# Kernel optimization log

Hardware: AMD Instinct MI355X
Metric: run time of the kernel (lower is better)

Reference implementation:

```python
import jax, jax.numpy as jnp
import numpy as np

B, T, C = 4, 2048, 1024
H, D = 16, 64  # num_heads, head_dim
WINDOW = 256


def setup_inputs() -> dict:
    key = jax.random.key(0)
    k_x, k_qkv, k_proj, k_qb, k_pb = jax.random.split(key, 5)
    x = jax.random.normal(k_x, (B, T, C), dtype=jnp.float32)
    # xavier-uniform-ish init for qkv weight (as in _reset_parameters)
    lim_qkv = float(np.sqrt(6.0 / (C + 3 * C)))
    qkv_w = jax.random.uniform(k_qkv, (3 * C, C), minval=-lim_qkv, maxval=lim_qkv, dtype=jnp.float32)
    qkv_b = jax.random.normal(k_qb, (3 * C,), dtype=jnp.float32) * 0.02
    lim_p = float(np.sqrt(1.0 / C))
    proj_w = jax.random.uniform(k_proj, (C, C), minval=-lim_p, maxval=lim_p, dtype=jnp.float32)
    proj_b = jax.random.normal(k_pb, (C,), dtype=jnp.float32) * 0.02
    # windowed causal mask: attend to j iff j <= i and i - j < WINDOW
    i = jnp.arange(T)[:, None]
    j = jnp.arange(T)[None, :]
    attn_mask = (j <= i) & (i - j < WINDOW)  # [T, T] bool
    return {"x": x, "attn_mask": attn_mask, "qkv_w": qkv_w, "qkv_b": qkv_b,
            "proj_w": proj_w, "proj_b": proj_b}


def reference(x, attn_mask, qkv_w, qkv_b, proj_w, proj_b):
    qkv = (x @ qkv_w.T + qkv_b).reshape(B, T, 3, H, D)
    qkv = jnp.transpose(qkv, (2, 0, 3, 1, 4))
    q, k, v = qkv[0], qkv[1], qkv[2]
    scale = 1.0 / jnp.sqrt(jnp.asarray(D, dtype=q.dtype))
    scores = jnp.einsum('bhqd,bhkd->bhqk', q, k) * scale  # [B,H,T,T]
    neg = jnp.asarray(jnp.finfo(scores.dtype).min, dtype=scores.dtype)
    scores = jnp.where(attn_mask[None, None], scores, neg)
    attn = jax.nn.softmax(scores, axis=-1)
    out = jnp.einsum('bhqk,bhkd->bhqd', attn, v)  # [B,H,T,D]
    out = jnp.transpose(out, (0, 2, 1, 3)).reshape(B, T, C)
    out = out @ proj_w.T + proj_b
    return out
```

## Files before the change

kernel.cpp:

```cpp
#include <hip/hip_runtime.h>

#define BB 4
#define TT 2048
#define CC 1024
#define HH 16
#define DD 64
#define WIN 256

typedef __attribute__((ext_vector_type(8))) short short8;
typedef __attribute__((ext_vector_type(4))) float floatx4;
typedef unsigned short u16;

typedef __attribute__((address_space(3))) void lds_void;
typedef const __attribute__((address_space(1))) void g_void;

__device__ __forceinline__ void gl_lds16(const u16* g, u16* l) {
    __builtin_amdgcn_global_load_lds((g_void*)g, (lds_void*)l, 16, 0, 0);
}

__device__ __forceinline__ float bf2f(u16 u) {
    union { unsigned int i; float f; } v; v.i = ((unsigned int)u) << 16; return v.f;
}
__device__ __forceinline__ u16 f2bf(float f) {
    union { float f; unsigned int i; } v; v.f = f;
    unsigned int x = v.i;
    x += ((x >> 16) & 1u) + 0x7FFFu;
    return (u16)(x >> 16);
}

__global__ void cvt_all(const float* __restrict__ x, const float* __restrict__ qw,
                        const float* __restrict__ pw,
                        u16* __restrict__ xb, u16* __restrict__ wb, u16* __restrict__ pwb) {
    int bid = blockIdx.x;
    const float* src; u16* dst; int off;
    if (bid < 4096)      { src = x;  dst = xb;  off = bid; }
    else if (bid < 5632) { src = qw; dst = wb;  off = bid - 4096; }
    else                 { src = pw; dst = pwb; off = bid - 5632; }
    int i = (off * 256 + (int)threadIdx.x) * 8;
    float4 a = *(const float4*)(src + i);
    float4 b = *(const float4*)(src + i + 4);
    u16 o[8] = { f2bf(a.x), f2bf(a.y), f2bf(a.z), f2bf(a.w),
                 f2bf(b.x), f2bf(b.y), f2bf(b.z), f2bf(b.w) };
    *(uint4*)(dst + i) = *(const uint4*)o;
}


#define STG(s, t) do { const int ko = (t) * 32;                              \
        gl_lds16(gA0 + ko, &lA[s][wave * 512]);                              \
        gl_lds16(gA1 + ko, &lA[s][4096 + wave * 512]);                       \
        gl_lds16(gB0 + ko, &lB[s][wave * 512]); } while (0)
#define LDAB(s) do { _Pragma("unroll")                                       \
        for (int i = 0; i < 4; ++i)                                          \
            af[i] = *(const short8*)&lA[s][(wm * 4 + i) * 512 + rdoff];      \
        _Pragma("unroll")                                                    \
        for (int j = 0; j < 4; ++j)                                          \
            bf[j] = *(const short8*)&lB[s][(wn * 4 + j) * 512 + rdoff]; } while (0)
#define MM() do { __builtin_amdgcn_s_setprio(1); _Pragma("unroll")           \
        for (int i = 0; i < 4; ++i) { _Pragma("unroll")                      \
            for (int j = 0; j < 4; ++j)                                      \
                acc[i][j] = __builtin_amdgcn_mfma_f32_16x16x32_bf16(         \
                    af[i], bf[j], acc[i][j], 0, 0, 0); }                     \
        __builtin_amdgcn_s_setprio(0); } while (0)
#define BARX() do { asm volatile("" ::: "memory");                           \
        __builtin_amdgcn_s_barrier();                                        \
        asm volatile("" ::: "memory"); } while (0)
#define VM12() asm volatile("s_waitcnt vmcnt(12)" ::: "memory")

#define GEMM_BODY                                                            \
    const int K = CC;                                                        \
    __shared__ u16 lA[6][8192];                                              \
    __shared__ u16 lB[6][4096];                                              \
    const int tid = threadIdx.x;                                             \
    const int wave = tid >> 6, lane = tid & 63;                              \
    const int wm = wave >> 1, wn = wave & 1;                                 \
    const int quad = lane >> 4, l15 = lane & 15;                             \
    const int r0 = wave * 16 + (lane >> 2);                                  \
    const int r1 = r0 + 128;                                                 \
    const int c0 = (lane & 3) ^ ((r0 >> 1) & 3);                             \
    const u16* gA0 = Amat + (size_t)(bM + r0) * K + c0 * 8;                  \
    const u16* gA1 = Amat + (size_t)(bM + r1) * K + c0 * 8;                  \
    const u16* gB0 = Bw + (size_t)(bN + r0) * K + c0 * 8;                    \
    const int rdoff = l15 * 32 + ((quad ^ ((l15 >> 1) & 3)) * 8);            \
    floatx4 acc[4][4] = {};                                                  \
    STG(0, 0); STG(1, 1); STG(2, 2); STG(3, 3); STG(4, 4);                   \
    VM12(); BARX();                                                          \
    _Pragma("unroll")                                                        \
    for (int P = 0; P < 32; ++P) {                                           \
        short8 af[4], bf[4];                                                 \
        LDAB(P % 6);                                                         \
        STG((P + 5) % 6, (P + 5 < 32) ? (P + 5) : (P - 1));                  \
        VM12(); BARX(); MM(); BARX();                                        \
    }

__global__ __launch_bounds__(512, 2) void gemm_qkv(
    const u16* __restrict__ Amat, const u16* __restrict__ Bw,
    const float* __restrict__ bias,
    u16* __restrict__ Qb, u16* __restrict__ Kb, u16* __restrict__ Vb)
{
    const int raw = blockIdx.x;
    const int xcd = raw & 7;
    const int l   = raw >> 3;
    const int bM  = (xcd * 4 + (l & 3)) * 256;
    const int bN  = (l >> 2) * 128;

    GEMM_BODY

#pragma unroll
    for (int mf = 0; mf < 4; ++mf)
#pragma unroll
        for (int nf = 0; nf < 4; ++nf) {
            int col = bN + wn * 64 + nf * 16 + l15;
            float bv = bias[col];
            int which = col >> 10, rem = col & 1023;
            int h = rem >> 6, d = rem & 63;
            u16* dst = which == 0 ? Qb : (which == 1 ? Kb : Vb);
#pragma unroll
            for (int rg = 0; rg < 4; ++rg) {
                int row = bM + wm * 64 + mf * 16 + quad * 4 + rg;
                int b = row >> 11, t = row & 2047;
                float v = acc[mf][nf][rg] + bv;
                dst[(((size_t)(b * HH + h)) * TT + t) * DD + d] = f2bf(v);
            }
        }
}

__global__ __launch_bounds__(512, 2) void gemm_proj(
    const u16* __restrict__ Amat, const u16* __restrict__ Bw,
    const float* __restrict__ bias, float* __restrict__ Out)
{
    const int raw = blockIdx.x;
    const int xcd = raw & 7;
    const int l   = raw >> 3;
    const int bM  = (xcd * 4 + (l & 3)) * 256;
    const int bN  = (l >> 2) * 128;

    GEMM_BODY

#pragma unroll
    for (int mf = 0; mf < 4; ++mf)
#pragma unroll
        for (int nf = 0; nf < 4; ++nf) {
            int col = bN + wn * 64 + nf * 16 + l15;
            float bv = bias[col];
#pragma unroll
            for (int rg = 0; rg < 4; ++rg) {
                int row = bM + wm * 64 + mf * 16 + quad * 4 + rg;
                Out[(size_t)row * CC + col] = acc[mf][nf][rg] + bv;
            }
        }
}

#undef STG
#undef LDAB
#undef MM
#undef BARX
#undef VM12
#undef GEMM_BODY

__global__ __launch_bounds__(256) void attn_mfma(
    const u16* __restrict__ Qb, const u16* __restrict__ Kb, const u16* __restrict__ Vb,
    u16* __restrict__ Y)
{
    __shared__ u16 Ks[64][72];
    __shared__ u16 Vt[64][72];
    __shared__ u16 Ps[4][16][72];

    const int tid = threadIdx.x;
    const int wave = tid >> 6, lane = tid & 63;
    const int quad = lane >> 4, l15 = lane & 15;
    const int q0 = blockIdx.x * 64;
    const int bh = blockIdx.y;
    const int b = bh >> 4, h = bh & 15;
    const u16* Qp = Qb + (size_t)bh * TT * DD;
    const u16* Kp = Kb + (size_t)bh * TT * DD;
    const u16* Vp = Vb + (size_t)bh * TT * DD;
    const int qw = q0 + wave * 16;

    short8 qf[2];
    qf[0] = *(const short8*)&Qp[(size_t)(qw + l15) * DD + quad * 8];
    qf[1] = *(const short8*)&Qp[(size_t)(qw + l15) * DD + 32 + quad * 8];

    float m_i[4] = { -1e30f, -1e30f, -1e30f, -1e30f };
    float l_i[4] = { 0.f, 0.f, 0.f, 0.f };
    floatx4 Oacc[4] = {};

    const int kb = (q0 >= WIN) ? (q0 - WIN) : 0;
    for (int j0 = kb; j0 < q0 + 64; j0 += 64) {
        __syncthreads();
#pragma unroll
        for (int it = 0; it < 2; ++it) {
            int slot = tid + it * 256;
            int j = slot >> 3, c8 = (slot & 7) << 3;
            *(uint4*)&Ks[j][c8] = *(const uint4*)&Kp[(size_t)(j0 + j) * DD + c8];
        }
#pragma unroll
        for (int it = 0; it < 2; ++it) {
            int slot = tid + it * 256;
            int j = slot >> 3, d0 = (slot & 7) << 3;
            uint4 raw = *(const uint4*)&Vp[(size_t)(j0 + j) * DD + d0];
            const u16* u = (const u16*)&raw;
#pragma unroll
            for (int i = 0; i < 8; ++i) {
                int d = d0 + i;
                int col = (((j >> 3) ^ (d >> 3)) << 3) + (j & 7);
                Vt[d][col] = u[i];
            }
        }
        __syncthreads();

        floatx4 Sacc[4] = {};
#pragma unroll
        for (int nt = 0; nt < 4; ++nt) {
            short8 kf0 = *(const short8*)&Ks[nt * 16 + l15][quad * 8];
            short8 kf1 = *(const short8*)&Ks[nt * 16 + l15][32 + quad * 8];
            Sacc[nt] = __builtin_amdgcn_mfma_f32_16x16x32_bf16(qf[0], kf0, Sacc[nt], 0, 0, 0);
            Sacc[nt] = __builtin_amdgcn_mfma_f32_16x16x32_bf16(qf[1], kf1, Sacc[nt], 0, 0, 0);
        }

        float mc[4] = { -1e30f, -1e30f, -1e30f, -1e30f };
#pragma unroll
        for (int nt = 0; nt < 4; ++nt)
#pragma unroll
            for (int r = 0; r < 4; ++r) {
                int q = qw + quad * 4 + r;
                int j = j0 + nt * 16 + l15;
                float s = (j <= q && (q - j) < WIN) ? Sacc[nt][r] * 0.125f : -1e30f;
                Sacc[nt][r] = s;
                mc[r] = fmaxf(mc[r], s);
            }
#pragma unroll
        for (int m = 1; m < 16; m <<= 1)
#pragma unroll
            for (int r = 0; r < 4; ++r) mc[r] = fmaxf(mc[r], __shfl_xor(mc[r], m, 64));

        float alpha[4];
#pragma unroll
        for (int r = 0; r < 4; ++r) {
            float mn = fmaxf(m_i[r], mc[r]);
            alpha[r] = __expf(m_i[r] - mn);
            m_i[r] = mn;
        }
        float rs[4] = { 0.f, 0.f, 0.f, 0.f };
#pragma unroll
        for (int nt = 0; nt < 4; ++nt)
#pragma unroll
            for (int r = 0; r < 4; ++r) {
                float s = Sacc[nt][r];
                float p = (s > -1e29f) ? __expf(s - m_i[r]) : 0.f;
                Sacc[nt][r] = p;
                rs[r] += p;
            }
#pragma unroll
        for (int m = 1; m < 16; m <<= 1)
#pragma unroll
            for (int r = 0; r < 4; ++r) rs[r] += __shfl_xor(rs[r], m, 64);
#pragma unroll
        for (int r = 0; r < 4; ++r) l_i[r] = l_i[r] * alpha[r] + rs[r];
#pragma unroll
        for (int dt = 0; dt < 4; ++dt)
#pragma unroll
            for (int r = 0; r < 4; ++r) Oacc[dt][r] *= alpha[r];

#pragma unroll
        for (int nt = 0; nt < 4; ++nt)
#pragma unroll
            for (int r = 0; r < 4; ++r)
                Ps[wave][quad * 4 + r][nt * 16 + l15] = f2bf(Sacc[nt][r]);

#pragma unroll
        for (int ks = 0; ks < 2; ++ks) {
            short8 pf = *(const short8*)&Ps[wave][l15][ks * 32 + quad * 8];
#pragma unroll
            for (int dt = 0; dt < 4; ++dt) {
                int d = dt * 16 + l15;
                int col = (((ks * 4 + quad) ^ (d >> 3)) << 3);
                short8 vf = *(const short8*)&Vt[d][col];
                Oacc[dt] = __builtin_amdgcn_mfma_f32_16x16x32_bf16(pf, vf, Oacc[dt], 0, 0, 0);
            }
        }
    }

    float inv[4];
#pragma unroll
    for (int r = 0; r < 4; ++r) inv[r] = 1.f / l_i[r];
#pragma unroll
    for (int dt = 0; dt < 4; ++dt)
#pragma unroll
        for (int r = 0; r < 4; ++r) {
            int t = qw + quad * 4 + r;
            int d = dt * 16 + l15;
            Y[((size_t)b * TT + t) * CC + h * DD + d] = f2bf(Oacc[dt][r] * inv[r]);
        }
}

extern "C" void kernel_launch(void* const* d_in, const int* in_sizes, int n_in,
                              void* d_out, int out_size, void* d_ws, size_t ws_size,
                              hipStream_t stream) {
    const float* x      = (const float*)d_in[0];
    const float* qkv_w  = (const float*)d_in[2];
    const float* qkv_b  = (const float*)d_in[3];
    const float* proj_w = (const float*)d_in[4];
    const float* proj_b = (const float*)d_in[5];
    float* out = (float*)d_out;

    u16* xb  = (u16*)d_ws;
    u16* wb  = xb  + (size_t)8192 * 1024;
    u16* pwb = wb  + (size_t)3072 * 1024;
    u16* Qb  = pwb + (size_t)1024 * 1024;
    u16* Kb  = Qb  + (size_t)64 * 2048 * 64;
    u16* Vb  = Kb  + (size_t)64 * 2048 * 64;
    u16* Yb  = Vb  + (size_t)64 * 2048 * 64;

    cvt_all<<<6144, 256, 0, stream>>>(x, qkv_w, proj_w, xb, wb, pwb);
    gemm_qkv<<<768, 512, 0, stream>>>(xb, wb, qkv_b, Qb, Kb, Vb);
    attn_mfma<<<dim3(TT / 64, BB * HH), 256, 0, stream>>>(Qb, Kb, Vb, Yb);
    gemm_proj<<<256, 512, 0, stream>>>(Yb, pwb, proj_b, out);
}
```

Before: 243.2 us.

## Restructure GEMM core to double-buffered 64-wide K steps with wider QKV tiles

Replaces the 6-stage, 32-wide-K pipeline with a templated GEMM core that double-buffers 64-wide K chunks, split into two halves so A and B loads interleave with the MFMAs. Waves are arranged 2x4, and each wave computes 8 row fragments by NR column fragments. The QKV GEMM moves from 256x128 to 256x192 tiles and launches 512 blocks instead of 768, giving more reuse per tile and fewer blocks. The risks are more accumulator registers at 2 blocks per CU, a different LDS footprint, and a shallower prefetch depth that may expose memory latency.

```diff
diff --git a/kernel.cpp b/kernel.cpp
--- a/kernel.cpp
+++ b/kernel.cpp
@@ -44,118 +44,170 @@
     *(uint4*)(dst + i) = *(const uint4*)o;
 }
 
-
-#define STG(s, t) do { const int ko = (t) * 32;                              \
-        gl_lds16(gA0 + ko, &lA[s][wave * 512]);                              \
-        gl_lds16(gA1 + ko, &lA[s][4096 + wave * 512]);                       \
-        gl_lds16(gB0 + ko, &lB[s][wave * 512]); } while (0)
-#define LDAB(s) do { _Pragma("unroll")                                       \
-        for (int i = 0; i < 4; ++i)                                          \
-            af[i] = *(const short8*)&lA[s][(wm * 4 + i) * 512 + rdoff];      \
-        _Pragma("unroll")                                                    \
-        for (int j = 0; j < 4; ++j)                                          \
-            bf[j] = *(const short8*)&lB[s][(wn * 4 + j) * 512 + rdoff]; } while (0)
-#define MM() do { __builtin_amdgcn_s_setprio(1); _Pragma("unroll")           \
-        for (int i = 0; i < 4; ++i) { _Pragma("unroll")                      \
-            for (int j = 0; j < 4; ++j)                                      \
-                acc[i][j] = __builtin_amdgcn_mfma_f32_16x16x32_bf16(         \
-                    af[i], bf[j], acc[i][j], 0, 0, 0); }                     \
-        __builtin_amdgcn_s_setprio(0); } while (0)
+#define VM4()  asm volatile("s_waitcnt vmcnt(4)" ::: "memory")
 #define BARX() do { asm volatile("" ::: "memory");                           \
         __builtin_amdgcn_s_barrier();                                        \
         asm volatile("" ::: "memory"); } while (0)
-#define VM12() asm volatile("s_waitcnt vmcnt(12)" ::: "memory")
-
-#define GEMM_BODY                                                            \
-    const int K = CC;                                                        \
-    __shared__ u16 lA[6][8192];                                              \
-    __shared__ u16 lB[6][4096];                                              \
-    const int tid = threadIdx.x;                                             \
-    const int wave = tid >> 6, lane = tid & 63;                              \
-    const int wm = wave >> 1, wn = wave & 1;                                 \
-    const int quad = lane >> 4, l15 = lane & 15;                             \
-    const int r0 = wave * 16 + (lane >> 2);                                  \
-    const int r1 = r0 + 128;                                                 \
-    const int c0 = (lane & 3) ^ ((r0 >> 1) & 3);                             \
-    const u16* gA0 = Amat + (size_t)(bM + r0) * K + c0 * 8;                  \
-    const u16* gA1 = Amat + (size_t)(bM + r1) * K + c0 * 8;                  \
-    const u16* gB0 = Bw + (size_t)(bN + r0) * K + c0 * 8;                    \
-    const int rdoff = l15 * 32 + ((quad ^ ((l15 >> 1) & 3)) * 8);            \
-    floatx4 acc[4][4] = {};                                                  \
-    STG(0, 0); STG(1, 1); STG(2, 2); STG(3, 3); STG(4, 4);                   \
-    VM12(); BARX();                                                          \
-    _Pragma("unroll")                                                        \
-    for (int P = 0; P < 32; ++P) {                                           \
-        short8 af[4], bf[4];                                                 \
-        LDAB(P % 6);                                                         \
-        STG((P + 5) % 6, (P + 5 < 32) ? (P + 5) : (P - 1));                  \
-        VM12(); BARX(); MM(); BARX();                                        \
+
+template<int NR>
+__device__ __forceinline__ void gemm_core(
+    const u16* __restrict__ Amat, const u16* __restrict__ Bw,
+    int bM, int bN, u16* lA, u16* lB, floatx4 (&acc)[8][NR])
+{
+    const int K = CC;
+    const int tid = threadIdx.x;
+    const int wave = tid >> 6, lane = tid & 63;
+    const int wm = wave >> 2, wn = wave & 3;
+    const int quad = lane >> 4, l15 = lane & 15;
+
+    const u16* gA[4]; int dA[4];
+#pragma unroll
+    for (int j = 0; j < 4; ++j) {
+        int off = j * 8192 + tid * 16;
+        int kh  = off >> 14;
+        int o2  = off & 16383;
+        int row = (o2 >> 10) * 16 + ((o2 & 1023) >> 6);
+        int c   = ((o2 >> 4) & 3) ^ ((row >> 1) & 3);
+        gA[j] = Amat + (size_t)(bM + row) * K + kh * 32 + c * 8;
+        dA[j] = off >> 1;
     }
+    const u16* gB[NR]; int dB[NR];
+#pragma unroll
+    for (int j = 0; j < NR; ++j) {
+        int off = j * 8192 + tid * 16;
+        int kh  = (off >= NR * 4096) ? 1 : 0;
+        int o2  = off - kh * NR * 4096;
+        int row = (o2 >> 10) * 16 + ((o2 & 1023) >> 6);
+        int c   = ((o2 >> 4) & 3) ^ ((row >> 1) & 3);
+        gB[j] = Bw + (size_t)(bN + row) * K + kh * 32 + c * 8;
+        dB[j] = off >> 1;
+    }
+
+    const int rdoff = l15 * 32 + ((quad ^ ((l15 >> 1) & 3)) * 8);
+
+    short8 af[8], bf[NR];
+
+    auto stgA = [&](int buf, int t) {
+#pragma unroll
+        for (int j = 0; j < 4; ++j)
+            gl_lds16(gA[j] + t * 64, lA + buf * 16384 + dA[j]);
+    };
+    auto stgB = [&](int buf, int t) {
+#pragma unroll
+        for (int j = 0; j < NR; ++j)
+            gl_lds16(gB[j] + t * 64, lB + buf * (NR * 4096) + dB[j]);
+    };
+    auto lda = [&](int buf, int kh) {
+#pragma unroll
+        for (int i = 0; i < 8; ++i)
+            af[i] = *(const short8*)&lA[buf * 16384 + kh * 8192 + (wm * 8 + i) * 512 + rdoff];
+    };
+    auto ldb = [&](int buf, int kh) {
+#pragma unroll
+        for (int j = 0; j < NR; ++j)
+            bf[j] = *(const short8*)&lB[buf * (NR * 4096) + kh * (NR * 2048) + (wn * NR + j) * 512 + rdoff];
+    };
+    auto mm = [&]() {
+        __builtin_amdgcn_s_setprio(1);
+#pragma unroll
+        for (int i = 0; i < 8; ++i)
+#pragma unroll
+            for (int j = 0; j < NR; ++j)
+                acc[i][j] = __builtin_amdgcn_mfma_f32_16x16x32_bf16(af[i], bf[j], acc[i][j], 0, 0, 0);
+        __builtin_amdgcn_s_setprio(0);
+    };
+
+    stgA(0, 0); stgB(0, 0);
+
+    for (int ii = 0; ii < 8; ++ii) {
+        const int t1 = 2 * ii + 1;
+        const int t2 = (ii < 7) ? 2 * ii + 2 : 15;
+        stgA(1, t1); VM4(); BARX();
+        lda(0, 0); ldb(0, 0); mm();
+        stgB(1, t1);
+        lda(0, 1); ldb(0, 1); mm();
+        BARX();
+        stgA(0, t2); VM4(); BARX();
+        lda(1, 0); ldb(1, 0); mm();
+        stgB(0, t2);
+        lda(1, 1); ldb(1, 1); mm();
+        BARX();
+    }
+}
 
 __global__ __launch_bounds__(512, 2) void gemm_qkv(
     const u16* __restrict__ Amat, const u16* __restrict__ Bw,
     const float* __restrict__ bias,
     u16* __restrict__ Qb, u16* __restrict__ Kb, u16* __restrict__ Vb)
 {
+    __shared__ u16 lA[2 * 16384];
+    __shared__ u16 lB[2 * 12288];
+    const int raw = blockIdx.x;
+    const int xcd = raw & 7;
+    const int l   = raw >> 3;
+    const int bM  = (xcd * 4 + (l & 3)) * 256;
+    const int bN  = (l >> 2) * 192;
+
+    floatx4 acc[8][3] = {};
+    gemm_core<3>(Amat, Bw, bM, bN, lA, lB, acc);
+
+    const int tid = threadIdx.x;
+    const int wave = tid >> 6, lane = tid & 63;
+    const int wm = wave >> 2, wn = wave & 3;
+    const int quad = lane >> 4, l15 = lane & 15;
+
+#pragma unroll
+    for (int mf = 0; mf < 8; ++mf)
+#pragma unroll
+        for (int nf = 0; nf < 3; ++nf) {
+            int col = bN + wn * 48 + nf * 16 + l15;
+            float bv = bias[col];
+            int which = col >> 10, rem = col & 1023;
+            int h = rem >> 6, d = rem & 63;
+            u16* dst = which == 0 ? Qb : (which == 1 ? Kb : Vb);
+#pragma unroll
+            for (int rg = 0; rg < 4; ++rg) {
+                int row = bM + wm * 128 + mf * 16 + quad * 4 + rg;
+                int b = row >> 11, t = row & 2047;
+                float v = acc[mf][nf][rg] + bv;
+                dst[(((size_t)(b * HH + h)) * TT + t) * DD + d] = f2bf(v);
+            }
+        }
+}
+
+__global__ __launch_bounds__(512, 2) void gemm_proj(
+    const u16* __restrict__ Amat, const u16* __restrict__ Bw,
+    const float* __restrict__ bias, float* __restrict__ Out)
+{
+    __shared__ u16 lA[2 * 16384];
+    __shared__ u16 lB[2 * 8192];
     const int raw = blockIdx.x;
     const int xcd = raw & 7;
     const int l   = raw >> 3;
     const int bM  = (xcd * 4 + (l & 3)) * 256;
     const int bN  = (l >> 2) * 128;
 
-    GEMM_BODY
-
-#pragma unroll
-    for (int mf = 0; mf < 4; ++mf)
-#pragma unroll
-        for (int nf = 0; nf < 4; ++nf) {
-            int col = bN + wn * 64 + nf * 16 + l15;
+    floatx4 acc[8][2] = {};
+    gemm_core<2>(Amat, Bw, bM, bN, lA, lB, acc);
+
+    const int tid = threadIdx.x;
+    const int wave = tid >> 6, lane = tid & 63;
+    const int wm = wave >> 2, wn = wave & 3;
+    const int quad = lane >> 4, l15 = lane & 15;
+
+#pragma unroll
+    for (int mf = 0; mf < 8; ++mf)
+#pragma unroll
+        for (int nf = 0; nf < 2; ++nf) {
+            int col = bN + wn * 32 + nf * 16 + l15;
             float bv = bias[col];
-            int which = col >> 10, rem = col & 1023;
-            int h = rem >> 6, d = rem & 63;
-            u16* dst = which == 0 ? Qb : (which == 1 ? Kb : Vb);
 #pragma unroll
             for (int rg = 0; rg < 4; ++rg) {
-                int row = bM + wm * 64 + mf * 16 + quad * 4 + rg;
-                int b = row >> 11, t = row & 2047;
-                float v = acc[mf][nf][rg] + bv;
-                dst[(((size_t)(b * HH + h)) * TT + t) * DD + d] = f2bf(v);
-            }
-        }
-}
-
-__global__ __launch_bounds__(512, 2) void gemm_proj(
-    const u16* __restrict__ Amat, const u16* __restrict__ Bw,
-    const float* __restrict__ bias, float* __restrict__ Out)
-{
-    const int raw = blockIdx.x;
-    const int xcd = raw & 7;
-    const int l   = raw >> 3;
-    const int bM  = (xcd * 4 + (l & 3)) * 256;
-    const int bN  = (l >> 2) * 128;
-
-    GEMM_BODY
-
-#pragma unroll
-    for (int mf = 0; mf < 4; ++mf)
-#pragma unroll
-        for (int nf = 0; nf < 4; ++nf) {
-            int col = bN + wn * 64 + nf * 16 + l15;
-            float bv = bias[col];
-#pragma unroll
-            for (int rg = 0; rg < 4; ++rg) {
-                int row = bM + wm * 64 + mf * 16 + quad * 4 + rg;
+                int row = bM + wm * 128 + mf * 16 + quad * 4 + rg;
                 Out[(size_t)row * CC + col] = acc[mf][nf][rg] + bv;
             }
         }
 }
-
-#undef STG
-#undef LDAB
-#undef MM
-#undef BARX
-#undef VM12
-#undef GEMM_BODY
 
 __global__ __launch_bounds__(256) void attn_mfma(
     const u16* __restrict__ Qb, const u16* __restrict__ Kb, const u16* __restrict__ Vb,
@@ -312,7 +364,7 @@
     u16* Yb  = Vb  + (size_t)64 * 2048 * 64;
 
     cvt_all<<<6144, 256, 0, stream>>>(x, qkv_w, proj_w, xb, wb, pwb);
-    gemm_qkv<<<768, 512, 0, stream>>>(xb, wb, qkv_b, Qb, Kb, Vb);
+    gemm_qkv<<<512, 512, 0, stream>>>(xb, wb, qkv_b, Qb, Kb, Vb);
     attn_mfma<<<dim3(TT / 64, BB * HH), 256, 0, stream>>>(Qb, Kb, Vb, Yb);
     gemm_proj<<<256, 512, 0, stream>>>(Yb, pwb, proj_b, out);
 }
```

New measurement: 234.9 us. -3.4%, faster.
